# Performance work log

Measured on AMD Instinct MI355X. Metric: run time of the kernel, lower is better.

## Reference

```python
import jax, jax.numpy as jnp
import numpy as np

B, C, H, W = 8, 3, 64, 64
HORIZON = 32
WIDTH = 32
M1 = M2 = M3 = 8
N_LAYERS = 4
C_OUT = 3


def setup_inputs() -> dict:
    key = jax.random.key(0)
    ks = jax.random.split(key, 16)
    scale = 1.0 / (WIDTH * WIDTH)
    wshape = (N_LAYERS, 4, WIDTH, WIDTH, M1, M2, M3)
    return {
        "x_t": jax.random.normal(ks[0], (B, C, H, W), dtype=jnp.float32),
        "p_w": jax.random.normal(ks[1], (WIDTH, C + 3), dtype=jnp.float32) * 0.1,
        "p_b": jnp.zeros((WIDTH,), dtype=jnp.float32),
        "spec_wr": scale * jax.random.normal(ks[2], wshape, dtype=jnp.float32),
        "spec_wi": scale * jax.random.normal(ks[3], wshape, dtype=jnp.float32),
        "pw_w": jax.random.normal(ks[4], (N_LAYERS, WIDTH, WIDTH), dtype=jnp.float32) * 0.1,
        "pw_b": jnp.zeros((N_LAYERS, WIDTH), dtype=jnp.float32),
        "q1_w": jax.random.normal(ks[5], (2 * WIDTH, WIDTH), dtype=jnp.float32) * 0.1,
        "q1_b": jnp.zeros((2 * WIDTH,), dtype=jnp.float32),
        "q2_w": jax.random.normal(ks[6], (C_OUT, 2 * WIDTH), dtype=jnp.float32) * 0.1,
        "q2_b": jnp.zeros((C_OUT,), dtype=jnp.float32),
        "horizon": HORIZON,
    }


def _conv1x1(x, w, b):
    # x: [b, i, x, y, z], w: [o, i] -> [b, o, x, y, z]
    return jnp.einsum("oi,bixyz->boxyz", w, x) + b[None, :, None, None, None]


def _spectral_conv3d(x, wr, wi):
    # x: [b, i, H, W, T]; wr/wi: [4, i, o, m1, m2, m3]
    h, w_, t = x.shape[-3], x.shape[-2], x.shape[-1]
    xf = jnp.fft.rfftn(x, axes=(-3, -2, -1))  # [b, i, H, W, T//2+1]
    wc = (wr + 1j * wi).astype(xf.dtype)
    m1 = min(M1, xf.shape[-3]); m2 = min(M2, xf.shape[-2]); m3 = min(M3, xf.shape[-1])
    mul = lambda a, ww: jnp.einsum("bixyz,ioxyz->boxyz", a, ww)
    out = jnp.zeros((x.shape[0], wr.shape[2]) + xf.shape[2:], dtype=xf.dtype)
    out = out.at[:, :, :m1, :m2, :m3].set(mul(xf[:, :, :m1, :m2, :m3], wc[0, :, :, :m1, :m2, :m3]))
    out = out.at[:, :, -m1:, :m2, :m3].set(mul(xf[:, :, -m1:, :m2, :m3], wc[1, :, :, :m1, :m2, :m3]))
    out = out.at[:, :, :m1, -m2:, :m3].set(mul(xf[:, :, :m1, -m2:, :m3], wc[2, :, :, :m1, :m2, :m3]))
    out = out.at[:, :, -m1:, -m2:, :m3].set(mul(xf[:, :, -m1:, -m2:, :m3], wc[3, :, :, :m1, :m2, :m3]))
    return jnp.fft.irfftn(out, s=(h, w_, t), axes=(-3, -2, -1))


def _grid_3d(b, h, w, t, dtype):
    gy = jnp.broadcast_to(jnp.linspace(0.0, 1.0, h, dtype=dtype)[None, None, :, None, None], (b, 1, h, w, t))
    gx = jnp.broadcast_to(jnp.linspace(0.0, 1.0, w, dtype=dtype)[None, None, None, :, None], (b, 1, h, w, t))
    gt = jnp.broadcast_to(jnp.linspace(0.0, 1.0, t, dtype=dtype)[None, None, None, None, :], (b, 1, h, w, t))
    return jnp.concatenate([gy, gx, gt], axis=1)


def reference(x_t, p_w, p_b, spec_wr, spec_wi, pw_w, pw_b, q1_w, q1_b, q2_w, q2_b, horizon):
    b, c, h, w = x_t.shape
    x = jnp.broadcast_to(x_t[..., None], (b, c, h, w, horizon))  # repeat over time
    grid = _grid_3d(b, h, w, horizon, x_t.dtype)
    x = jnp.concatenate([x, grid], axis=1)  # [b, c+3, h, w, t]
    x = _conv1x1(x, p_w, p_b)
    for l in range(N_LAYERS):
        x = jax.nn.gelu(
            _spectral_conv3d(x, spec_wr[l], spec_wi[l]) + _conv1x1(x, pw_w[l], pw_b[l]),
            approximate=False,
        )
    x = _conv1x1(x, q1_w, q1_b)
    x = jax.nn.gelu(x, approximate=False)
    x = _conv1x1(x, q2_w, q2_b)
    # [b, c_out, h, w, t] -> [b, t, c_out, h, w]
    return jnp.transpose(x, (0, 4, 1, 2, 3))
```

## Files before the change

### kernel.cpp

```cpp
#include <hip/hip_runtime.h>
#include <math.h>


#define TWO_PI 6.2831853071795864769f

typedef short bf16x8 __attribute__((ext_vector_type(8)));
typedef float f32x4 __attribute__((ext_vector_type(4)));
typedef float v2f __attribute__((ext_vector_type(2)));

__device__ __forceinline__ f32x4 mfma16(bf16x8 a, bf16x8 b, f32x4 c) {
    return __builtin_amdgcn_mfma_f32_16x16x32_bf16(a, b, c, 0, 0, 0);
}

__device__ __forceinline__ void split8(float4 a, float4 b, bf16x8& h, bf16x8& l) {
    float f[8] = {a.x, a.y, a.z, a.w, b.x, b.y, b.z, b.w};
    #pragma unroll
    for (int i = 0; i < 8; ++i) {
        unsigned u = __float_as_uint(f[i]);
        h[i] = (short)(u >> 16);
        float hf = __uint_as_float(u & 0xFFFF0000u);
        float lf = f[i] - hf;
        l[i] = (short)(__float_as_uint(lf) >> 16);
    }
}

__device__ __forceinline__ unsigned packhl(float f) {
    unsigned u = __float_as_uint(f);
    unsigned hi = u & 0xFFFF0000u;
    float lf = f - __uint_as_float(hi);
    return hi | (__float_as_uint(lf) >> 16);
}

__device__ __forceinline__ void unpack8(uint4 a, uint4 b, bf16x8& h, bf16x8& l) {
    unsigned u[8] = {a.x, a.y, a.z, a.w, b.x, b.y, b.z, b.w};
    #pragma unroll
    for (int i = 0; i < 8; ++i) {
        h[i] = (short)(u[i] >> 16);
        l[i] = (short)(u[i] & 0xFFFFu);
    }
}

__device__ __forceinline__ v2f make2(float x) { v2f r; r.x = x; r.y = x; return r; }
__device__ __forceinline__ v2f fma2(v2f a, v2f b, v2f c) { return __builtin_elementwise_fma(a, b, c); }

__device__ __forceinline__ v2f gelu2(v2f v) {
    v2f u = v * 0.70710678118654752f;
    v2f a = __builtin_elementwise_abs(u);
    v2f den = fma2(a, make2(0.3275911f), make2(1.0f));
    v2f t; t.x = __builtin_amdgcn_rcpf(den.x); t.y = __builtin_amdgcn_rcpf(den.y);
    v2f p = t * (0.254829592f + t * (-0.284496736f + t * (1.421413741f +
            t * (-1.453152027f + t * 1.061405429f))));
    v2f e; e.x = __expf(-u.x * u.x); e.y = __expf(-u.y * u.y);
    v2f m = fma2(-p, e, make2(1.0f));
    v2f erfu = __builtin_elementwise_copysign(m, u);
    return 0.5f * v * (1.0f + erfu);
}

__device__ __forceinline__ void gelu4(f32x4& q) {
    v2f p0; p0.x = q[0]; p0.y = q[1];
    v2f p1; p1.x = q[2]; p1.y = q[3];
    p0 = gelu2(p0); p1 = gelu2(p1);
    q[0] = p0.x; q[1] = p0.y; q[2] = p1.x; q[3] = p1.y;
}

__device__ __forceinline__ void make_fwd_A(int l15, int quad, bf16x8& Gh, bf16x8& Gl) {
    int k = l15 >> 1;
    float s0, c0, ds, dc;
    __sincosf((float)(k * quad * 8) * (TWO_PI / 32.0f), &s0, &c0);
    __sincosf((float)k * (TWO_PI / 32.0f), &ds, &dc);
    float m[8];
    float cc = c0, ss = s0;
    #pragma unroll
    for (int j = 0; j < 8; ++j) {
        m[j] = (l15 & 1) ? -ss : cc;
        float nc = cc * dc - ss * ds;
        float ns = ss * dc + cc * ds;
        cc = nc; ss = ns;
    }
    split8(make_float4(m[0], m[1], m[2], m[3]),
           make_float4(m[4], m[5], m[6], m[7]), Gh, Gl);
}

__device__ __forceinline__ void fwd_tdft(const unsigned* up, int b, int sp0,
                                         float2* __restrict__ T1,
                                         int wb, int l15, int quad,
                                         bf16x8 Gh, bf16x8 Gl) {
    #pragma unroll
    for (int nt = 0; nt < 4; ++nt) {
        int r = wb + nt * 16 + l15;
        const uint4* p = (const uint4*)(up + r * 36 + quad * 8);
        bf16x8 bh, bl; unpack8(p[0], p[1], bh, bl);
        f32x4 d = {0.f, 0.f, 0.f, 0.f};
        d = mfma16(Gh, bh, d);
        d = mfma16(Gl, bh, d);
        d = mfma16(Gh, bl, d);
        int c = r & 31, spl = r >> 5;
        float4* ob = (float4*)(T1 + ((long)(b * 32 + c) * 4096 + sp0 + spl) * 8 + quad * 2);
        *ob = make_float4(d[0], d[1], d[2], d[3]);
    }
}

__device__ __forceinline__ void make_invx_A(int x0, int l15, int quad, bf16x8& Ah, bf16x8& Al) {
    int spl = l15 >> 1, ro = l15 & 1;
    float xx = (float)(x0 + spl);
    const float S = 1.0f / 131072.0f;
    float f[8];
    #pragma unroll
    for (int m = 0; m < 4; ++m) {
        int kxi = quad * 4 + m;
        float kx = (float)(kxi < 8 ? kxi : kxi - 16);
        float sn, cs;
        __sincosf(kx * xx * (TWO_PI / 64.0f), &sn, &cs);
        f[2 * m]     = ro ? S * sn : S * cs;
        f[2 * m + 1] = ro ? S * cs : -S * sn;
    }
    split8(make_float4(f[0], f[1], f[2], f[3]),
           make_float4(f[4], f[5], f[6], f[7]), Ah, Al);
}

__device__ __forceinline__ void invx_reg(float* smem, const float2 v[4], int half, int wave,
                                         int nt2, int l15, int quad, bf16x8 xAh, bf16x8 xAl) {
    float f[8];
    #pragma unroll
    for (int m = 0; m < 4; ++m) { f[2 * m] = v[m].x; f[2 * m + 1] = v[m].y; }
    bf16x8 bh, bl;
    split8(make_float4(f[0], f[1], f[2], f[3]),
           make_float4(f[4], f[5], f[6], f[7]), bh, bl);
    f32x4 d = {0.f, 0.f, 0.f, 0.f};
    d = mfma16(xAh, bh, d);
    d = mfma16(xAl, bh, d);
    d = mfma16(xAh, bl, d);
    int ol = (wave * 2 + nt2) * 2 + (l15 >> 3), kt = l15 & 7;
    int o = half * 16 + ol;
    #pragma unroll
    for (int reg = 0; reg < 4; ++reg) {
        int m_ = quad * 4 + reg, spl = m_ >> 1, ri = m_ & 1;
        smem[o * 132 + spl * 16 + kt * 2 + ri] = d[reg];
    }
}

__global__ __launch_bounds__(256) void k_lift(const float* __restrict__ xt,
                                              const float* __restrict__ pw,
                                              const float* __restrict__ pb,
                                              unsigned* __restrict__ X,
                                              float2* __restrict__ T1) {
    __shared__ unsigned xs[9216];
    int gg = blockIdx.x;
    int g = ((gg & 7) << 9) | (gg >> 3);
    int spt = g & 511, b = g >> 9;
    int sp0 = spt * 8;
    int y = sp0 >> 6, x0 = sp0 & 63;
    int tid = threadIdx.x;
    int t = tid & 31, spl = tid >> 5;
    int sp = sp0 + spl;
    float a0 = xt[(b * 3 + 0) * 4096 + sp];
    float a1 = xt[(b * 3 + 1) * 4096 + sp];
    float a2 = xt[(b * 3 + 2) * 4096 + sp];
    float gy = y * (1.0f / 63.0f), gx = (x0 + spl) * (1.0f / 63.0f), gt = t * (1.0f / 31.0f);
    float v[32];
    #pragma unroll
    for (int c = 0; c < 32; ++c) {
        const float* w = pw + c * 6;
        v[c] = pb[c] + w[0] * a0 + w[1] * a1 + w[2] * a2
             + w[3] * gy + w[4] * gx + w[5] * gt;
    }
    unsigned pk[32];
    #pragma unroll
    for (int c = 0; c < 32; ++c) pk[c] = packhl(v[c]);
    unsigned* xg2 = X + (((long)(b * 4096 + sp)) * 32 + t) * 32;
    #pragma unroll
    for (int j = 0; j < 8; ++j)
        ((uint4*)xg2)[j] = make_uint4(pk[4*j], pk[4*j+1], pk[4*j+2], pk[4*j+3]);
    #pragma unroll
    for (int c = 0; c < 32; ++c)
        xs[(spl * 32 + c) * 36 + t] = pk[c];
    int wave = tid >> 6, lane = tid & 63, l15 = lane & 15, quad = lane >> 4;
    bf16x8 Gh, Gl; make_fwd_A(l15, quad, Gh, Gl);
    __syncthreads();
    fwd_tdft(xs, b, sp0, T1, wave * 64, l15, quad, Gh, Gl);
}

__global__ __launch_bounds__(256) void k_xdft(const float2* __restrict__ T1, float2* __restrict__ T2) {
    __shared__ float2 s[1024];
    __shared__ float2 tw[64];
    int g = blockIdx.x;
    int ypair = g & 31; int bc = g >> 5;
    long base = ((long)bc * 64 + ypair * 2) * 512;
    int tid = threadIdx.x;
    for (int k = tid; k < 1024; k += 256) s[k] = T1[base + k];
    if (tid < 64) { float sn, cs; __sincosf(tid * (TWO_PI / 64.0f), &sn, &cs); tw[tid] = make_float2(cs, sn); }
    __syncthreads();
    #pragma unroll
    for (int r = 0; r < 2; ++r) {
        int j = tid + r * 256;
        int half = j >> 8, rem = j & 255;
        int idx = half * 512 + rem;
        float2 a = s[idx], b2 = s[idx + 256];
        s[idx] = make_float2(a.x + b2.x, a.y + b2.y);
        s[idx + 256] = make_float2(a.x - b2.x, a.y - b2.y);
    }
    __syncthreads();
    int half = tid >> 7, jj = tid & 127;
    int kxi = jj >> 3, kt = jj & 7;
    int kx = kxi < 8 ? kxi : kxi + 48;
    const float2* row = s + half * 512 + (kx & 1) * 256;
    float sr = 0.f, si = 0.f;
    for (int x = 0; x < 32; ++x) {
        float2 w = tw[(kx * x) & 63];
        float2 a = row[x * 8 + kt];
        sr += a.x * w.x + a.y * w.y;
        si += a.y * w.x - a.x * w.y;
    }
    T2[((long)bc * 64 + ypair * 2 + half) * 128 + jj] = make_float2(sr, si);
}

__global__ __launch_bounds__(128) void k_ydft(const float2* __restrict__ T2, float2* __restrict__ T3) {
    __shared__ float2 s[512];
    __shared__ float2 tw[64];
    int g = blockIdx.x;
    int kx = g & 15; int bc = g >> 4;
    int tid = threadIdx.x;
    for (int k = tid; k < 512; k += 128) {
        int y = k >> 3, kt = k & 7;
        s[k] = T2[((long)bc * 64 + y) * 128 + kx * 8 + kt];
    }
    if (tid < 64) { float sn, cs; __sincosf(tid * (TWO_PI / 64.0f), &sn, &cs); tw[tid] = make_float2(cs, sn); }
    __syncthreads();
    #pragma unroll
    for (int r = 0; r < 2; ++r) {
        int j = tid + r * 128;
        float2 a = s[j], b2 = s[j + 256];
        s[j] = make_float2(a.x + b2.x, a.y + b2.y);
        s[j + 256] = make_float2(a.x - b2.x, a.y - b2.y);
    }
    __syncthreads();
    int kyi = tid >> 3, kt = tid & 7;
    int ky = kyi < 8 ? kyi : kyi + 48;
    const float2* row = s + (ky & 1) * 256;
    float sr = 0.f, si = 0.f;
    for (int y = 0; y < 32; ++y) {
        float2 w = tw[(ky * y) & 63];
        float2 a = row[y * 8 + kt];
        sr += a.x * w.x + a.y * w.y;
        si += a.y * w.x - a.x * w.y;
    }
    T3[((long)bc * 256 + kyi * 16 + kx) * 8 + kt] = make_float2(sr, si);
}

__global__ __launch_bounds__(256) void k_mix2(const float2* __restrict__ T3,
                                              const float* __restrict__ wr,
                                              const float* __restrict__ wi,
                                              float2* __restrict__ T4, int layer) {
    __shared__ float2 s[2304];
    int mode = blockIdx.x;
    int kyi = mode >> 4, kxi = mode & 15;
    int tid = threadIdx.x;
    {
        int bb = tid >> 5, i = tid & 31;
        const float2* src = T3 + ((long)(bb * 32 + i) * 256 + mode) * 8;
        float2* dst = s + (i * 8 + bb) * 9;
        #pragma unroll
        for (int k = 0; k < 8; ++k) dst[k] = src[k];
    }
    __syncthreads();
    int corner = (kyi >= 8 ? 1 : 0) + (kxi >= 8 ? 2 : 0);
    long wbase = (long)(layer * 4 + corner) * 524288 + (long)(kyi & 7) * 64 + (long)(kxi & 7) * 8;
    int o = tid >> 3, kt = tid & 7;
    long wb = wbase + (long)o * 512 + kt;
    float2 acc[8];
    #pragma unroll
    for (int bb = 0; bb < 8; ++bb) acc[bb] = make_float2(0.f, 0.f);
    for (int i = 0; i < 32; ++i) {
        float r = wr[wb + (long)i * 16384], im = wi[wb + (long)i * 16384];
        #pragma unroll
        for (int bb = 0; bb < 8; ++bb) {
            float2 a = s[(i * 8 + bb) * 9 + kt];
            acc[bb].x += a.x * r - a.y * im;
            acc[bb].y += a.x * im + a.y * r;
        }
    }
    #pragma unroll
    for (int bb = 0; bb < 8; ++bb)
        T4[((long)(bb * 32 + o) * 256 + mode) * 8 + kt] = acc[bb];
}

__global__ __launch_bounds__(256) void k_invy(const float2* __restrict__ T4, float2* __restrict__ T5) {
    __shared__ float2 s[128];
    __shared__ float2 tw[64];
    __shared__ float2 pmP[56], pmM[56];
    int g = blockIdx.x;
    int kx = g & 15; int bc = g >> 4;
    int tid = threadIdx.x;
    if (tid < 128) {
        int kyi = tid >> 3, kt = tid & 7;
        s[tid] = T4[((long)bc * 256 + kyi * 16 + kx) * 8 + kt];
    } else if (tid < 192) {
        int m = tid - 128; float sn, cs; __sincosf(m * (TWO_PI / 64.0f), &sn, &cs); tw[m] = make_float2(cs, sn);
    }
    __syncthreads();
    if (tid < 56) {
        int j = (tid >> 3) + 1, kt = tid & 7;
        float2 a = s[j * 8 + kt], b2 = s[(16 - j) * 8 + kt];
        pmP[tid] = make_float2(a.x + b2.x, a.y + b2.y);
        pmM[tid] = make_float2(a.x - b2.x, a.y - b2.y);
    }
    __syncthreads();
    #pragma unroll
    for (int r = 0; r < 2; ++r) {
        int j = tid + r * 256;
        int y = j >> 3, kt = j & 7;
        float2 A0 = s[kt], A8 = s[64 + kt];
        float2 w8 = tw[(8 * y) & 63];
        float sr = A0.x + A8.x * w8.x + A8.y * w8.y;
        float si = A0.y + A8.y * w8.x - A8.x * w8.y;
        #pragma unroll
        for (int jj = 1; jj < 8; ++jj) {
            float2 w = tw[(jj * y) & 63];
            float2 P = pmP[(jj - 1) * 8 + kt], M = pmM[(jj - 1) * 8 + kt];
            sr += P.x * w.x - M.y * w.y;
            si += P.y * w.x + M.x * w.y;
        }
        T5[((long)bc * 64 + y) * 128 + kx * 8 + kt] = make_float2(sr, si);
    }
}

__device__ __forceinline__ void make_invt_A(int l15, int quad, bf16x8 Ah[2], bf16x8 Al[2]) {
    #pragma unroll
    for (int th = 0; th < 2; ++th) {
        float m[8];
        if (quad < 2) {
            int tt = th * 16 + l15;
            #pragma unroll
            for (int kk = 0; kk < 4; ++kk) {
                int k = quad * 4 + kk;
                float sn, cs;
                __sincosf((float)(k * tt) * (TWO_PI / 32.0f), &sn, &cs);
                float w = k ? 2.0f : 1.0f;
                m[2 * kk] = w * cs;
                m[2 * kk + 1] = -w * sn;
            }
        } else {
            #pragma unroll
            for (int j = 0; j < 8; ++j) m[j] = 0.f;
        }
        split8(make_float4(m[0], m[1], m[2], m[3]),
               make_float4(m[4], m[5], m[6], m[7]), Ah[th], Al[th]);
    }
}

__global__ __launch_bounds__(256) void k_fuse3(unsigned* __restrict__ X, const float2* __restrict__ T5,
                                               const float* __restrict__ pww,
                                               const float* __restrict__ pwb,
                                               float2* __restrict__ T1, int layer) {
    __shared__ float smem[9216];
    int gg = blockIdx.x;
    int g = ((gg & 7) << 9) | (gg >> 3);
    int spt = g & 511, b = g >> 9;
    int sp0 = spt * 8;
    int y = sp0 >> 6, x0 = sp0 & 63;
    int tid = threadIdx.x;
    int wave = tid >> 6, lane = tid & 63, l15 = lane & 15, quad = lane >> 4;
    int wb = wave * 64;
    float2 t5v[2][2][4];
    #pragma unroll
    for (int half = 0; half < 2; ++half)
        #pragma unroll
        for (int nt2 = 0; nt2 < 2; ++nt2) {
            int ol = (wave * 2 + nt2) * 2 + (l15 >> 3);
            const float2* rp = T5 + ((long)((b * 32 + half * 16 + ol) * 64 + y)) * 128 + (l15 & 7);
            #pragma unroll
            for (int m = 0; m < 4; ++m)
                t5v[half][nt2][m] = rp[(quad * 4 + m) * 8];
        }
    const float* wl = pww + layer * 1024;
    const float* bl = pwb + layer * 32;
    bf16x8 wah[2], wal[2];
    f32x4 acc[2][4];
    #pragma unroll
    for (int mt = 0; mt < 2; ++mt) {
        const float4* p = (const float4*)(wl + (mt * 16 + l15) * 32 + quad * 8);
        split8(p[0], p[1], wah[mt], wal[mt]);
        float4 bv = *(const float4*)(bl + mt * 16 + quad * 4);
        f32x4 bi; bi[0] = bv.x; bi[1] = bv.y; bi[2] = bv.z; bi[3] = bv.w;
        #pragma unroll
        for (int nt = 0; nt < 4; ++nt) acc[mt][nt] = bi;
    }
    #pragma unroll
    for (int nt = 0; nt < 4; ++nt) {
        int pt = wb + nt * 16 + l15;
        int spl = pt >> 5, t = pt & 31;
        const uint4* xp = (const uint4*)(X + (((long)(b * 4096 + sp0 + spl)) * 32 + t) * 32 + quad * 8);
        bf16x8 bh, blo; unpack8(xp[0], xp[1], bh, blo);
        #pragma unroll
        for (int mt = 0; mt < 2; ++mt) {
            acc[mt][nt] = mfma16(wah[mt], bh, acc[mt][nt]);
            acc[mt][nt] = mfma16(wal[mt], bh, acc[mt][nt]);
            acc[mt][nt] = mfma16(wah[mt], blo, acc[mt][nt]);
        }
    }
    bf16x8 Ah[2], Al[2];
    make_invt_A(l15, quad, Ah, Al);
    bf16x8 xAh, xAl;
    make_invx_A(x0, l15, quad, xAh, xAl);
    #pragma unroll
    for (int half = 0; half < 2; ++half)
        #pragma unroll
        for (int nt2 = 0; nt2 < 2; ++nt2)
            invx_reg(smem, t5v[half][nt2], half, wave, nt2, l15, quad, xAh, xAl);
    __syncthreads();
    bf16x8 Bh[2][2], Bl[2][2];
    #pragma unroll
    for (int sph = 0; sph < 2; ++sph) {
        int spl = 2 * wave + sph;
        #pragma unroll
        for (int ch = 0; ch < 2; ++ch) {
            float4 q0 = make_float4(0.f, 0.f, 0.f, 0.f), q1 = q0;
            if (quad < 2) {
                const float4* p = (const float4*)((float2*)smem + (ch * 16 + l15) * 66 + spl * 8 + quad * 4);
                q0 = p[0]; q1 = p[1];
            }
            split8(q0, q1, Bh[sph][ch], Bl[sph][ch]);
        }
    }
    __syncthreads();
    #pragma unroll
    for (int sph = 0; sph < 2; ++sph)
        #pragma unroll
        for (int ch = 0; ch < 2; ++ch)
            #pragma unroll
            for (int th = 0; th < 2; ++th) {
                int nt = sph * 2 + th;
                acc[ch][nt] = mfma16(Bh[sph][ch], Ah[th], acc[ch][nt]);
                acc[ch][nt] = mfma16(Bl[sph][ch], Ah[th], acc[ch][nt]);
                acc[ch][nt] = mfma16(Bh[sph][ch], Al[th], acc[ch][nt]);
            }
    bf16x8 Gh, Gl; make_fwd_A(l15, quad, Gh, Gl);
    #pragma unroll
    for (int mt = 0; mt < 2; ++mt)
        #pragma unroll
        for (int nt = 0; nt < 4; ++nt) gelu4(acc[mt][nt]);
    unsigned* up = (unsigned*)smem;
    #pragma unroll
    for (int mt = 0; mt < 2; ++mt)
        #pragma unroll
        for (int nt = 0; nt < 4; ++nt) {
            int pt = wb + nt * 16 + l15;
            int spl = pt >> 5, t = pt & 31;
            int o0 = mt * 16 + quad * 4;
            unsigned pk0 = packhl(acc[mt][nt][0]), pk1 = packhl(acc[mt][nt][1]);
            unsigned pk2 = packhl(acc[mt][nt][2]), pk3 = packhl(acc[mt][nt][3]);
            *(uint4*)(X + (((long)(b * 4096 + sp0 + spl)) * 32 + t) * 32 + o0) =
                make_uint4(pk0, pk1, pk2, pk3);
            up[(spl * 32 + o0 + 0) * 36 + t] = pk0;
            up[(spl * 32 + o0 + 1) * 36 + t] = pk1;
            up[(spl * 32 + o0 + 2) * 36 + t] = pk2;
            up[(spl * 32 + o0 + 3) * 36 + t] = pk3;
        }
    __syncthreads();
    fwd_tdft(up, b, sp0, T1, wb, l15, quad, Gh, Gl);
}

__global__ __launch_bounds__(256) void k_fuse3_last(const unsigned* __restrict__ X, const float2* __restrict__ T5,
                                                    const float* __restrict__ pww, const float* __restrict__ pwb,
                                                    const float* __restrict__ q1w, const float* __restrict__ q1b,
                                                    const float* __restrict__ q2w, const float* __restrict__ q2b,
                                                    float* __restrict__ out) {
    __shared__ float smem[9408];
    int gg = blockIdx.x;
    int g = ((gg & 7) << 9) | (gg >> 3);
    int spt = g & 511, b = g >> 9;
    int sp0 = spt * 8;
    int y = sp0 >> 6, x0 = sp0 & 63;
    int tid = threadIdx.x;
    int wave = tid >> 6, lane = tid & 63, l15 = lane & 15, quad = lane >> 4;
    int wb = wave * 64;
    float2 t5v[2][2][4];
    #pragma unroll
    for (int half = 0; half < 2; ++half)
        #pragma unroll
        for (int nt2 = 0; nt2 < 2; ++nt2) {
            int ol = (wave * 2 + nt2) * 2 + (l15 >> 3);
            const float2* rp = T5 + ((long)((b * 32 + half * 16 + ol) * 64 + y)) * 128 + (l15 & 7);
            #pragma unroll
            for (int m = 0; m < 4; ++m)
                t5v[half][nt2][m] = rp[(quad * 4 + m) * 8];
        }
    if (tid < 192) smem[9216 + tid] = q2w[tid];
    const float* wl = pww + 3 * 1024;
    const float* bl = pwb + 3 * 32;
    bf16x8 wah[2], wal[2];
    f32x4 acc[2][4];
    #pragma unroll
    for (int mt = 0; mt < 2; ++mt) {
        const float4* p = (const float4*)(wl + (mt * 16 + l15) * 32 + quad * 8);
        split8(p[0], p[1], wah[mt], wal[mt]);
        float4 bv = *(const float4*)(bl + mt * 16 + quad * 4);
        f32x4 bi; bi[0] = bv.x; bi[1] = bv.y; bi[2] = bv.z; bi[3] = bv.w;
        #pragma unroll
        for (int nt = 0; nt < 4; ++nt) acc[mt][nt] = bi;
    }
    #pragma unroll
    for (int nt = 0; nt < 4; ++nt) {
        int pt = wb + nt * 16 + l15;
        int spl = pt >> 5, t = pt & 31;
        const uint4* xp = (const uint4*)(X + (((long)(b * 4096 + sp0 + spl)) * 32 + t) * 32 + quad * 8);
        bf16x8 bh, blo; unpack8(xp[0], xp[1], bh, blo);
        #pragma unroll
        for (int mt = 0; mt < 2; ++mt) {
            acc[mt][nt] = mfma16(wah[mt], bh, acc[mt][nt]);
            acc[mt][nt] = mfma16(wal[mt], bh, acc[mt][nt]);
            acc[mt][nt] = mfma16(wah[mt], blo, acc[mt][nt]);
        }
    }
    bf16x8 Ah[2], Al[2];
    make_invt_A(l15, quad, Ah, Al);
    bf16x8 xAh, xAl;
    make_invx_A(x0, l15, quad, xAh, xAl);
    #pragma unroll
    for (int half = 0; half < 2; ++half)
        #pragma unroll
        for (int nt2 = 0; nt2 < 2; ++nt2)
            invx_reg(smem, t5v[half][nt2], half, wave, nt2, l15, quad, xAh, xAl);
    __syncthreads();
    bf16x8 Bh[2][2], Bl[2][2];
    #pragma unroll
    for (int sph = 0; sph < 2; ++sph) {
        int spl = 2 * wave + sph;
        #pragma unroll
        for (int ch = 0; ch < 2; ++ch) {
            float4 q0 = make_float4(0.f, 0.f, 0.f, 0.f), q1 = q0;
            if (quad < 2) {
                const float4* p = (const float4*)((float2*)smem + (ch * 16 + l15) * 66 + spl * 8 + quad * 4);
                q0 = p[0]; q1 = p[1];
            }
            split8(q0, q1, Bh[sph][ch], Bl[sph][ch]);
        }
    }
    __syncthreads();
    #pragma unroll
    for (int sph = 0; sph < 2; ++sph)
        #pragma unroll
        for (int ch = 0; ch < 2; ++ch)
            #pragma unroll
            for (int th = 0; th < 2; ++th) {
                int nt = sph * 2 + th;
                acc[ch][nt] = mfma16(Bh[sph][ch], Ah[th], acc[ch][nt]);
                acc[ch][nt] = mfma16(Bl[sph][ch], Ah[th], acc[ch][nt]);
                acc[ch][nt] = mfma16(Bh[sph][ch], Al[th], acc[ch][nt]);
            }
    #pragma unroll
    for (int mt = 0; mt < 2; ++mt)
        #pragma unroll
        for (int nt = 0; nt < 4; ++nt) gelu4(acc[mt][nt]);
    unsigned* up = (unsigned*)smem;
    #pragma unroll
    for (int mt = 0; mt < 2; ++mt)
        #pragma unroll
        for (int nt = 0; nt < 4; ++nt) {
            int pt = wb + nt * 16 + l15;
            int o0 = mt * 16 + quad * 4;
            *(uint4*)(up + pt * 36 + o0) =
                make_uint4(packhl(acc[mt][nt][0]), packhl(acc[mt][nt][1]),
                           packhl(acc[mt][nt][2]), packhl(acc[mt][nt][3]));
        }
    __syncthreads();
    bf16x8 qah[4], qal[4];
    f32x4 qbv[4];
    #pragma unroll
    for (int mt = 0; mt < 4; ++mt) {
        const float4* p = (const float4*)(q1w + (mt * 16 + l15) * 32 + quad * 8);
        split8(p[0], p[1], qah[mt], qal[mt]);
        float4 bv = *(const float4*)(q1b + mt * 16 + quad * 4);
        qbv[mt][0] = bv.x; qbv[mt][1] = bv.y; qbv[mt][2] = bv.z; qbv[mt][3] = bv.w;
    }
    const float* q2l = smem + 9216;
    float q2b0 = q2b[0], q2b1 = q2b[1], q2b2 = q2b[2];
    float oc0[4], oc1[4], oc2[4];
    #pragma unroll
    for (int nt = 0; nt < 4; ++nt) {
        int pt = wb + nt * 16 + l15;
        const uint4* bp = (const uint4*)(up + pt * 36 + quad * 8);
        bf16x8 bh, blo; unpack8(bp[0], bp[1], bh, blo);
        float p0 = 0.f, p1 = 0.f, p2 = 0.f;
        #pragma unroll
        for (int mt = 0; mt < 4; ++mt) {
            f32x4 h = qbv[mt];
            h = mfma16(qah[mt], bh, h);
            h = mfma16(qal[mt], bh, h);
            h = mfma16(qah[mt], blo, h);
            gelu4(h);
            #pragma unroll
            for (int reg = 0; reg < 4; ++reg) {
                int hh = mt * 16 + quad * 4 + reg;
                p0 += q2l[hh] * h[reg];
                p1 += q2l[64 + hh] * h[reg];
                p2 += q2l[128 + hh] * h[reg];
            }
        }
        p0 += __shfl_xor(p0, 16); p0 += __shfl_xor(p0, 32);
        p1 += __shfl_xor(p1, 16); p1 += __shfl_xor(p1, 32);
        p2 += __shfl_xor(p2, 16); p2 += __shfl_xor(p2, 32);
        oc0[nt] = p0 + q2b0; oc1[nt] = p1 + q2b1; oc2[nt] = p2 + q2b2;
    }
    __syncthreads();
    if (quad == 0) {
        #pragma unroll
        for (int nt = 0; nt < 4; ++nt) {
            int pt = wb + nt * 16 + l15;
            int spl = pt >> 5, t = pt & 31;
            smem[(t * 3 + 0) * 9 + spl] = oc0[nt];
            smem[(t * 3 + 1) * 9 + spl] = oc1[nt];
            smem[(t * 3 + 2) * 9 + spl] = oc2[nt];
        }
    }
    __syncthreads();
    for (int m = tid; m < 768; m += 256) {
        int u = m >> 3, spl = m & 7;
        out[((long)(b * 96 + u)) * 4096 + sp0 + spl] = smem[u * 9 + spl];
    }
}

extern "C" void kernel_launch(void* const* d_in, const int* in_sizes, int n_in,
                              void* d_out, int out_size, void* d_ws, size_t ws_size,
                              hipStream_t stream) {
    const float* xt  = (const float*)d_in[0];
    const float* pw  = (const float*)d_in[1];
    const float* pb  = (const float*)d_in[2];
    const float* swr = (const float*)d_in[3];
    const float* swi = (const float*)d_in[4];
    const float* pww = (const float*)d_in[5];
    const float* pwb = (const float*)d_in[6];
    const float* q1w = (const float*)d_in[7];
    const float* q1b = (const float*)d_in[8];
    const float* q2w = (const float*)d_in[9];
    const float* q2b = (const float*)d_in[10];
    float* out = (float*)d_out;

    unsigned* X  = (unsigned*)d_ws;
    float2* T1 = (float2*)((float*)d_ws + 33554432);
    float2* T2 = (float2*)((float*)T1 + 16777216);
    float2* T3 = (float2*)((float*)T2 + 4194304);
    float2* T4 = (float2*)((float*)T3 + 1048576);

    k_lift<<<4096, 256, 0, stream>>>(xt, pw, pb, X, T1);
    for (int l = 0; l < 4; ++l) {
        k_xdft<<<8192, 256, 0, stream>>>(T1, T2);
        k_ydft<<<4096, 128, 0, stream>>>(T2, T3);
        k_mix2<<<256, 256, 0, stream>>>(T3, swr, swi, T4, l);
        k_invy<<<4096, 256, 0, stream>>>(T4, T2);
        if (l < 3)
            k_fuse3<<<4096, 256, 0, stream>>>(X, T2, pww, pwb, T1, l);
        else
            k_fuse3_last<<<4096, 256, 0, stream>>>(X, T2, pww, pwb, q1w, q1b, q2w, q2b, out);
    }
}
```

Baseline: 685.3 us.

## Split mix kernel over batch, vectorize DFT loads, pre-split inverse-y output to bf16 pairs

Changes k_mix2 to launch four times as many blocks, each handling two batch entries instead of eight, which shrinks shared memory and registers and improves occupancy across the GPU. The k_xdft and k_ydft global-to-shared loads now use float4 vectors. k_invy writes its output already packed as bf16 high/low pairs, so k_fuse3 unpacks it instead of splitting floats. The trade-off is that each spectral weight is now reloaded by four blocks, and the packed format relies on the existing packhl/unpack8 helpers matching split8 exactly.

```diff
diff --git a/kernel.cpp b/kernel.cpp
--- a/kernel.cpp
+++ b/kernel.cpp
@@ -118,14 +118,11 @@
            make_float4(f[4], f[5], f[6], f[7]), Ah, Al);
 }
 
-__device__ __forceinline__ void invx_reg(float* smem, const float2 v[4], int half, int wave,
+__device__ __forceinline__ void invx_reg(float* smem, const uint2 v[4], int half, int wave,
                                          int nt2, int l15, int quad, bf16x8 xAh, bf16x8 xAl) {
-    float f[8];
-    #pragma unroll
-    for (int m = 0; m < 4; ++m) { f[2 * m] = v[m].x; f[2 * m + 1] = v[m].y; }
-    bf16x8 bh, bl;
-    split8(make_float4(f[0], f[1], f[2], f[3]),
-           make_float4(f[4], f[5], f[6], f[7]), bh, bl);
+    uint4 a = make_uint4(v[0].x, v[0].y, v[1].x, v[1].y);
+    uint4 b = make_uint4(v[2].x, v[2].y, v[3].x, v[3].y);
+    bf16x8 bh, bl; unpack8(a, b, bh, bl);
     f32x4 d = {0.f, 0.f, 0.f, 0.f};
     d = mfma16(xAh, bh, d);
     d = mfma16(xAl, bh, d);
@@ -187,7 +184,12 @@
     int ypair = g & 31; int bc = g >> 5;
     long base = ((long)bc * 64 + ypair * 2) * 512;
     int tid = threadIdx.x;
-    for (int k = tid; k < 1024; k += 256) s[k] = T1[base + k];
+    {
+        float4* s4 = (float4*)s;
+        const float4* src4 = (const float4*)(T1 + base);
+        #pragma unroll
+        for (int r = 0; r < 2; ++r) s4[tid + r * 256] = src4[tid + r * 256];
+    }
     if (tid < 64) { float sn, cs; __sincosf(tid * (TWO_PI / 64.0f), &sn, &cs); tw[tid] = make_float2(cs, sn); }
     __syncthreads();
     #pragma unroll
@@ -220,9 +222,14 @@
     int g = blockIdx.x;
     int kx = g & 15; int bc = g >> 4;
     int tid = threadIdx.x;
-    for (int k = tid; k < 512; k += 128) {
-        int y = k >> 3, kt = k & 7;
-        s[k] = T2[((long)bc * 64 + y) * 128 + kx * 8 + kt];
+    {
+        float4* s4 = (float4*)s;
+        #pragma unroll
+        for (int r = 0; r < 2; ++r) {
+            int k = tid + r * 128;
+            int y = k >> 2, j = k & 3;
+            s4[k] = ((const float4*)(T2 + ((long)bc * 64 + y) * 128 + kx * 8))[j];
+        }
     }
     if (tid < 64) { float sn, cs; __sincosf(tid * (TWO_PI / 64.0f), &sn, &cs); tw[tid] = make_float2(cs, sn); }
     __syncthreads();
@@ -251,40 +258,40 @@
                                               const float* __restrict__ wr,
                                               const float* __restrict__ wi,
                                               float2* __restrict__ T4, int layer) {
-    __shared__ float2 s[2304];
-    int mode = blockIdx.x;
+    __shared__ float2 s[576];
+    int g = blockIdx.x;
+    int bbh = g & 3, mode = g >> 2;
     int kyi = mode >> 4, kxi = mode & 15;
     int tid = threadIdx.x;
-    {
-        int bb = tid >> 5, i = tid & 31;
-        const float2* src = T3 + ((long)(bb * 32 + i) * 256 + mode) * 8;
-        float2* dst = s + (i * 8 + bb) * 9;
-        #pragma unroll
-        for (int k = 0; k < 8; ++k) dst[k] = src[k];
+    #pragma unroll
+    for (int r = 0; r < 2; ++r) {
+        int k = tid + r * 256;
+        int i = k >> 4, bbl = (k >> 3) & 1, kt = k & 7;
+        s[(i * 2 + bbl) * 9 + kt] =
+            T3[((long)((bbh * 2 + bbl) * 32 + i) * 256 + mode) * 8 + kt];
     }
     __syncthreads();
     int corner = (kyi >= 8 ? 1 : 0) + (kxi >= 8 ? 2 : 0);
     long wbase = (long)(layer * 4 + corner) * 524288 + (long)(kyi & 7) * 64 + (long)(kxi & 7) * 8;
     int o = tid >> 3, kt = tid & 7;
     long wb = wbase + (long)o * 512 + kt;
-    float2 acc[8];
-    #pragma unroll
-    for (int bb = 0; bb < 8; ++bb) acc[bb] = make_float2(0.f, 0.f);
+    float2 acc[2];
+    acc[0] = make_float2(0.f, 0.f); acc[1] = make_float2(0.f, 0.f);
     for (int i = 0; i < 32; ++i) {
         float r = wr[wb + (long)i * 16384], im = wi[wb + (long)i * 16384];
         #pragma unroll
-        for (int bb = 0; bb < 8; ++bb) {
-            float2 a = s[(i * 8 + bb) * 9 + kt];
-            acc[bb].x += a.x * r - a.y * im;
-            acc[bb].y += a.x * im + a.y * r;
-        }
-    }
-    #pragma unroll
-    for (int bb = 0; bb < 8; ++bb)
-        T4[((long)(bb * 32 + o) * 256 + mode) * 8 + kt] = acc[bb];
-}
-
-__global__ __launch_bounds__(256) void k_invy(const float2* __restrict__ T4, float2* __restrict__ T5) {
+        for (int bbl = 0; bbl < 2; ++bbl) {
+            float2 a = s[(i * 2 + bbl) * 9 + kt];
+            acc[bbl].x += a.x * r - a.y * im;
+            acc[bbl].y += a.x * im + a.y * r;
+        }
+    }
+    #pragma unroll
+    for (int bbl = 0; bbl < 2; ++bbl)
+        T4[((long)((bbh * 2 + bbl) * 32 + o) * 256 + mode) * 8 + kt] = acc[bbl];
+}
+
+__global__ __launch_bounds__(256) void k_invy(const float2* __restrict__ T4, uint2* __restrict__ T5) {
     __shared__ float2 s[128];
     __shared__ float2 tw[64];
     __shared__ float2 pmP[56], pmM[56];
@@ -320,7 +327,7 @@
             sr += P.x * w.x - M.y * w.y;
             si += P.y * w.x + M.x * w.y;
         }
-        T5[((long)bc * 64 + y) * 128 + kx * 8 + kt] = make_float2(sr, si);
+        T5[((long)bc * 64 + y) * 128 + kx * 8 + kt] = make_uint2(packhl(sr), packhl(si));
     }
 }
 
@@ -348,7 +355,7 @@
     }
 }
 
-__global__ __launch_bounds__(256) void k_fuse3(unsigned* __restrict__ X, const float2* __restrict__ T5,
+__global__ __launch_bounds__(256) void k_fuse3(unsigned* __restrict__ X, const uint2* __restrict__ T5,
                                                const float* __restrict__ pww,
                                                const float* __restrict__ pwb,
                                                float2* __restrict__ T1, int layer) {
@@ -361,13 +368,13 @@
     int tid = threadIdx.x;
     int wave = tid >> 6, lane = tid & 63, l15 = lane & 15, quad = lane >> 4;
     int wb = wave * 64;
-    float2 t5v[2][2][4];
+    uint2 t5v[2][2][4];
     #pragma unroll
     for (int half = 0; half < 2; ++half)
         #pragma unroll
         for (int nt2 = 0; nt2 < 2; ++nt2) {
             int ol = (wave * 2 + nt2) * 2 + (l15 >> 3);
-            const float2* rp = T5 + ((long)((b * 32 + half * 16 + ol) * 64 + y)) * 128 + (l15 & 7);
+            const uint2* rp = T5 + ((long)((b * 32 + half * 16 + ol) * 64 + y)) * 128 + (l15 & 7);
             #pragma unroll
             for (int m = 0; m < 4; ++m)
                 t5v[half][nt2][m] = rp[(quad * 4 + m) * 8];
@@ -460,7 +467,7 @@
     fwd_tdft(up, b, sp0, T1, wb, l15, quad, Gh, Gl);
 }
 
-__global__ __launch_bounds__(256) void k_fuse3_last(const unsigned* __restrict__ X, const float2* __restrict__ T5,
+__global__ __launch_bounds__(256) void k_fuse3_last(const unsigned* __restrict__ X, const uint2* __restrict__ T5,
                                                     const float* __restrict__ pww, const float* __restrict__ pwb,
                                                     const float* __restrict__ q1w, const float* __restrict__ q1b,
                                                     const float* __restrict__ q2w, const float* __restrict__ q2b,
@@ -474,13 +481,13 @@
     int tid = threadIdx.x;
     int wave = tid >> 6, lane = tid & 63, l15 = lane & 15, quad = lane >> 4;
     int wb = wave * 64;
-    float2 t5v[2][2][4];
+    uint2 t5v[2][2][4];
     #pragma unroll
     for (int half = 0; half < 2; ++half)
         #pragma unroll
         for (int nt2 = 0; nt2 < 2; ++nt2) {
             int ol = (wave * 2 + nt2) * 2 + (l15 >> 3);
-            const float2* rp = T5 + ((long)((b * 32 + half * 16 + ol) * 64 + y)) * 128 + (l15 & 7);
+            const uint2* rp = T5 + ((long)((b * 32 + half * 16 + ol) * 64 + y)) * 128 + (l15 & 7);
             #pragma unroll
             for (int m = 0; m < 4; ++m)
                 t5v[half][nt2][m] = rp[(quad * 4 + m) * 8];
@@ -646,11 +653,11 @@
     for (int l = 0; l < 4; ++l) {
         k_xdft<<<8192, 256, 0, stream>>>(T1, T2);
         k_ydft<<<4096, 128, 0, stream>>>(T2, T3);
-        k_mix2<<<256, 256, 0, stream>>>(T3, swr, swi, T4, l);
-        k_invy<<<4096, 256, 0, stream>>>(T4, T2);
+        k_mix2<<<1024, 256, 0, stream>>>(T3, swr, swi, T4, l);
+        k_invy<<<4096, 256, 0, stream>>>(T4, (uint2*)T2);
         if (l < 3)
-            k_fuse3<<<4096, 256, 0, stream>>>(X, T2, pww, pwb, T1, l);
+            k_fuse3<<<4096, 256, 0, stream>>>(X, (const uint2*)T2, pww, pwb, T1, l);
         else
-            k_fuse3_last<<<4096, 256, 0, stream>>>(X, T2, pww, pwb, q1w, q1b, q2w, q2b, out);
-    }
-}
+            k_fuse3_last<<<4096, 256, 0, stream>>>(X, (const uint2*)T2, pww, pwb, q1w, q1b, q2w, q2b, out);
+    }
+}
```

Result: slower. 713.4 us (+4.1%).
